# Kernel optimization log

Measured on AMD Instinct MI355X. Metric: run time of the kernel, lower is better.

Reference implementation:

```python
import jax, jax.numpy as jnp
import numpy as np

K = 1024
D = 256
BETA = 0.25


def setup_inputs() -> dict:
    key = jax.random.key(0)
    k1, k2 = jax.random.split(key)
    latents = jax.random.normal(k1, (32, D, 32, 32), dtype=jnp.float32)
    # nn.Embedding init: uniform(-1/K, 1/K)
    embedding = jax.random.uniform(k2, (K, D), dtype=jnp.float32,
                                   minval=-1.0 / K, maxval=1.0 / K)
    return {"latents": latents, "embedding": embedding}


def reference(latents, embedding):
    # latents: [B, D, H, W] -> [B, H, W, D]
    x = jnp.transpose(latents, (0, 2, 3, 1))
    input_shape = x.shape
    flat = x.reshape(-1, D)  # [N, D]

    # squared-L2 distances to codebook: [N, K]
    distances = (jnp.sum(flat ** 2, axis=1, keepdims=True)
                 + jnp.sum(embedding ** 2, axis=1)
                 - 2.0 * flat @ embedding.T)
    encoding_indices = jnp.argmin(distances, axis=1)  # [N]

    # one-hot encodings (returned output); quantize via direct gather
    encodings = jax.nn.one_hot(encoding_indices, K, dtype=latents.dtype)  # [N, K]
    quantized = embedding[encoding_indices].reshape(input_shape)  # [B, H, W, D]

    e_latent_loss = jnp.mean((jax.lax.stop_gradient(quantized) - x) ** 2)
    q_latent_loss = jnp.mean((quantized - jax.lax.stop_gradient(x)) ** 2)
    loss = q_latent_loss + BETA * e_latent_loss

    # straight-through estimator
    quantized_st = x + jax.lax.stop_gradient(quantized - x)

    avg_probs = jnp.mean(encodings, axis=0)  # [K]
    perplexity = jnp.exp(-jnp.sum(avg_probs * jnp.log(avg_probs + 1e-10)))

    return (loss,
            jnp.transpose(quantized_st, (0, 3, 1, 2)),  # [B, D, H, W]
            perplexity,
            encodings)
```

## Files before the change

kernel.cpp:

```cpp
#include <hip/hip_runtime.h>
#include <stdint.h>
#include <math.h>

typedef float  f32x4 __attribute__((ext_vector_type(4)));
typedef float  f32x2 __attribute__((ext_vector_type(2)));
typedef short  s16x8 __attribute__((ext_vector_type(8)));
typedef short  s16x4 __attribute__((ext_vector_type(4)));

#define KC   1024
#define DD   256
#define NR   32768

#define WS_HIST   0
#define WS_ACC    4096
#define WS_E2     8192
#define WS_IDX    12288
#define WS_PANEL  143360

#define ENC_OFF   8388610ULL

#define A_OFF   0
#define B_OFF   32768
#define E2_OFF  49152
#define SMEM_SZ 53248

#define GLD16(gp, lp) __builtin_amdgcn_global_load_lds(                      \
    (const __attribute__((address_space(1))) uint32_t*)(gp),                 \
    (__attribute__((address_space(3))) uint32_t*)(lp), 16, 0, 0)

__device__ __forceinline__ short f2bf(float f) {
    uint32_t u = __builtin_bit_cast(uint32_t, f);
    uint32_t r = (u + 0x7FFFu + ((u >> 16) & 1u)) >> 16;
    return (short)r;
}

__global__ void k_prep(const float* __restrict__ emb, char* __restrict__ ws) {
    int tid = threadIdx.x;
    if (blockIdx.x == 0) {
        uint32_t* hist = (uint32_t*)(ws + WS_HIST);
        #pragma unroll
        for (int j = 0; j < 4; j++) hist[tid * 4 + j] = 0u;
        if (tid < 2) ((float*)(ws + WS_ACC))[tid] = 0.f;
    }
    int wid = tid >> 6, lane = tid & 63;
    int code = blockIdx.x * 4 + wid;
    const float* row = emb + (size_t)code * DD;
    f32x4 v = *(const f32x4*)(row + lane * 4);
    s16x4 b;
    b[0] = f2bf(v.x); b[1] = f2bf(v.y); b[2] = f2bf(v.z); b[3] = f2bf(v.w);
    *(s16x4*)((short*)(ws + WS_PANEL) + (size_t)code * DD + lane * 4) = b;
    float ss = v.x * v.x + v.y * v.y + v.z * v.z + v.w * v.w;
    #pragma unroll
    for (int off = 1; off < 64; off <<= 1) ss += __shfl_xor(ss, off);
    if (lane == 0) ((float*)(ws + WS_E2))[code] = ss;
}

__global__ __launch_bounds__(256, 3) void k_argmin(const float* __restrict__ latents,
                                                   char* __restrict__ ws) {
    const char*  panelb = (const char*)(ws + WS_PANEL);
    const float* e2g    = (const float*)(ws + WS_E2);
    uint32_t*    hist   = (uint32_t*)(ws + WS_HIST);
    float*       acc    = (float*)(ws + WS_ACC);
    int*         idxo   = (int*)(ws + WS_IDX);

    __shared__ __align__(16) char smem[SMEM_SZ];

    int t    = threadIdx.x;
    int lane = t & 63;
    int wid  = t >> 6;
    int g    = lane >> 4, r16 = lane & 15;
    int nbase  = blockIdx.x * 128;
    int b      = nbase >> 10;
    int hwbase = nbase & 1023;

    #pragma unroll
    for (int i = 0; i < 2; i++) {
        uint32_t off = i * 4096 + wid * 1024;
        uint32_t so  = off + lane * 16;
        uint32_t ssw = so ^ (((so >> 9) & 7u) << 4);
        GLD16(panelb + ssw, smem + B_OFF + off);
    }
    {
        f32x4 ev = *(const f32x4*)(e2g + t * 4);
        *(f32x4*)(smem + E2_OFF + t * 16) = ev;
    }

    float xs = 0.f;
    s16x8 af[2][8];
    int rg = (t & 15) * 4;
    int dp = (t >> 4) * 2;
    int wb = 4 * ((t >> 4) & 3);

    #pragma unroll
    for (int h = 0; h < 2; h++) {
        const float* base = latents + (size_t)b * 262144 + hwbase + h * 64 + rg;
        #pragma unroll
        for (int i = 0; i < 8; i++) {
            int d = dp + i * 32;
            f32x4 v0 = *(const f32x4*)(base + (size_t)d * 1024);
            f32x4 v1 = *(const f32x4*)(base + (size_t)(d + 1) * 1024);
            xs += v0.x*v0.x + v0.y*v0.y + v0.z*v0.z + v0.w*v0.w;
            xs += v1.x*v1.x + v1.y*v1.y + v1.z*v1.z + v1.w*v1.w;
            int qb = d >> 3;
            #pragma unroll
            for (int q = 0; q < 4; q++) {
                int slot = rg + q;
                uint32_t pk = (uint32_t)(uint16_t)f2bf(v0[q])
                            | ((uint32_t)(uint16_t)f2bf(v1[q]) << 16);
                int quad = qb ^ (slot & 7);
                *(uint32_t*)(smem + A_OFF + slot * 512 + quad * 16 + wb) = pk;
            }
        }
        __syncthreads();
        if ((wid >> 1) == h) {
            int slotbase = (wid & 1) * 32;
            #pragma unroll
            for (int rt = 0; rt < 2; rt++) {
                #pragma unroll
                for (int kt = 0; kt < 8; kt++) {
                    int slot = slotbase + rt * 16 + r16;
                    int quad = (kt * 4 + g) ^ (slot & 7);
                    af[rt][kt] = *(const s16x8*)(smem + A_OFF + slot * 512 + quad * 16);
                }
            }
        }
        __syncthreads();
    }
    #pragma unroll
    for (int off = 1; off < 64; off <<= 1) xs += __shfl_xor(xs, off);
    if (lane == 0) atomicAdd(acc + 0, xs);
    __syncthreads();

    float vmin[2][4];
    int   vidx[2][4];
    #pragma unroll
    for (int rt = 0; rt < 2; rt++)
        #pragma unroll
        for (int j = 0; j < 4; j++) { vmin[rt][j] = 3.4e38f; vidx[rt][j] = 0; }

    const float* E2l = (const float*)(smem + E2_OFF);
    int cur = 0;
    for (int c = 0; c < 64; ++c) {
        if (c < 63) {
            size_t srcc = (size_t)(c + 1) * 8192;
            #pragma unroll
            for (int i = 0; i < 2; i++) {
                uint32_t off = i * 4096 + wid * 1024;
                uint32_t so  = off + lane * 16;
                uint32_t ssw = so ^ (((so >> 9) & 7u) << 4);
                GLD16(panelb + srcc + ssw, smem + B_OFF + (cur ^ 1) * 8192 + off);
            }
        }
        int cbase = c * 16;
        float e2c = E2l[cbase + r16];
        const char* Bc = smem + B_OFF + cur * 8192;
        s16x8 bf[8];
        #pragma unroll
        for (int kt = 0; kt < 8; kt++) {
            uint32_t byte = (uint32_t)(r16 * 512) + (((uint32_t)(kt * 64 + g * 16)) ^ (((uint32_t)(r16 & 7)) << 4));
            bf[kt] = *(const s16x8*)(Bc + byte);
        }
        #pragma unroll
        for (int rt = 0; rt < 2; rt++) {
            f32x4 a4 = {0.f, 0.f, 0.f, 0.f};
            #pragma unroll
            for (int kt = 0; kt < 8; kt++)
                a4 = __builtin_amdgcn_mfma_f32_16x16x32_bf16(af[rt][kt], bf[kt], a4, 0, 0, 0);
            #pragma unroll
            for (int j = 0; j < 4; j++) {
                float s = e2c - 2.f * a4[j];
                bool better = s < vmin[rt][j];
                vmin[rt][j] = better ? s : vmin[rt][j];
                vidx[rt][j] = better ? (cbase + r16) : vidx[rt][j];
            }
        }
        __syncthreads();
        cur ^= 1;
    }

    float minsum = 0.f;
    #pragma unroll
    for (int rt = 0; rt < 2; rt++) {
        #pragma unroll
        for (int j = 0; j < 4; j++) {
            float s = vmin[rt][j]; int ii = vidx[rt][j];
            #pragma unroll
            for (int off = 1; off < 16; off <<= 1) {
                float os = __shfl_xor(s, off);
                int   oi = __shfl_xor(ii, off);
                if (os < s || (os == s && oi < ii)) { s = os; ii = oi; }
            }
            minsum += s;
            if (r16 == 0) {
                int n = nbase + wid * 32 + rt * 16 + g * 4 + j;
                idxo[n] = ii;
                atomicAdd(hist + ii, 1u);
            }
        }
    }
    minsum += __shfl_xor(minsum, 16);
    minsum += __shfl_xor(minsum, 32);
    if (lane == 0) atomicAdd(acc + 1, minsum);
}

__global__ void k_quant(const float* __restrict__ emb, const char* __restrict__ ws,
                        float* __restrict__ out) {
    const int* idx = (const int*)(ws + WS_IDX);
    int tid = threadIdx.x;
    int dg  = blockIdx.x & 63;
    int hwt = (blockIdx.x >> 6) & 3;
    int b   = blockIdx.x >> 8;
    int hw  = hwt * 256 + tid;
    int n   = b * 1024 + hw;
    int code = idx[n];
    f32x4 v = *(const f32x4*)(emb + (size_t)code * 256 + dg * 4);
    float* dst = out + 1 + (size_t)b * 262144 + (size_t)dg * 4096 + hw;
    dst[0] = v.x; dst[1024] = v.y; dst[2048] = v.z; dst[3072] = v.w;
}

__global__ void k_onehot(const char* __restrict__ ws, float* __restrict__ out) {
    const int* idx = (const int*)(ws + WS_IDX);
    __shared__ int lidx[8];
    int tid = threadIdx.x;
    int rbase = blockIdx.x * 8;
    if (tid < 8) lidx[tid] = idx[rbase + tid];
    __syncthreads();
    f32x2* enc = (f32x2*)(out + ENC_OFF);
    #pragma unroll
    for (int j = 0; j < 16; j++) {
        int linear = j * 256 + tid;
        int rl = linear >> 9, c2 = linear & 511;
        int id = lidx[rl];
        f32x2 v;
        v.x = (2 * c2     == id) ? 1.f : 0.f;
        v.y = (2 * c2 + 1 == id) ? 1.f : 0.f;
        enc[(size_t)(rbase + rl) * 512 + c2] = v;
    }
}

__global__ void k_final(const char* __restrict__ ws, float* __restrict__ out) {
    __shared__ float red[256];
    const uint32_t* hist = (const uint32_t*)(ws + WS_HIST);
    const float*    acc  = (const float*)(ws + WS_ACC);
    int tid = threadIdx.x;
    float part = 0.f;
    #pragma unroll
    for (int j = 0; j < 4; j++) {
        float p = (float)hist[tid * 4 + j] * (1.f / 32768.f);
        part += p * logf(p + 1e-10f);
    }
    red[tid] = part;
    __syncthreads();
    for (int s = 128; s > 0; s >>= 1) {
        if (tid < s) red[tid] += red[tid + s];
        __syncthreads();
    }
    if (tid == 0) {
        out[8388609] = expf(-red[0]);
        out[0] = 1.25f * (acc[0] + acc[1]) * (1.f / 8388608.f);
    }
}

extern "C" void kernel_launch(void* const* d_in, const int* in_sizes, int n_in,
                              void* d_out, int out_size, void* d_ws, size_t ws_size,
                              hipStream_t stream) {
    const float* latents = (const float*)d_in[0];
    const float* emb     = (const float*)d_in[1];
    float* out = (float*)d_out;
    char*  ws  = (char*)d_ws;

    hipLaunchKernelGGL(k_prep,   dim3(256),  dim3(256), 0, stream, emb, ws);
    hipLaunchKernelGGL(k_argmin, dim3(256),  dim3(256), 0, stream, latents, ws);
    hipLaunchKernelGGL(k_quant,  dim3(8192), dim3(256), 0, stream, emb, ws, out);
    hipLaunchKernelGGL(k_onehot, dim3(4096), dim3(256), 0, stream, ws, out);
    hipLaunchKernelGGL(k_final,  dim3(1),    dim3(256), 0, stream, ws, out);
}
```

Before: 109.8 us.

## Split argmin codebook scan across two blocks and combine partial minima

Doubles the argmin grid by giving each block half of the codebook for its 128 rows. Each block writes its partial (min distance, index) pairs to workspace, and a new combine kernel picks the winner, writes the indices, histogram and min-sum. This aims to fill more compute units and shorten the serial codebook loop per block. The cost is that latent rows are loaded and converted twice, plus an extra kernel launch and partial-result traffic.

```diff
diff --git a/kernel.cpp b/kernel.cpp
--- a/kernel.cpp
+++ b/kernel.cpp
@@ -16,13 +16,14 @@
 #define WS_E2     8192
 #define WS_IDX    12288
 #define WS_PANEL  143360
+#define WS_PART   671744
 
 #define ENC_OFF   8388610ULL
 
 #define A_OFF   0
 #define B_OFF   32768
 #define E2_OFF  49152
-#define SMEM_SZ 53248
+#define SMEM_SZ 51200
 
 #define GLD16(gp, lp) __builtin_amdgcn_global_load_lds(                      \
     (const __attribute__((address_space(1))) uint32_t*)(gp),                 \
@@ -55,33 +56,34 @@
     if (lane == 0) ((float*)(ws + WS_E2))[code] = ss;
 }
 
-__global__ __launch_bounds__(256, 3) void k_argmin(const float* __restrict__ latents,
+__global__ __launch_bounds__(256, 2) void k_argmin(const float* __restrict__ latents,
                                                    char* __restrict__ ws) {
     const char*  panelb = (const char*)(ws + WS_PANEL);
     const float* e2g    = (const float*)(ws + WS_E2);
-    uint32_t*    hist   = (uint32_t*)(ws + WS_HIST);
     float*       acc    = (float*)(ws + WS_ACC);
-    int*         idxo   = (int*)(ws + WS_IDX);
 
     __shared__ __align__(16) char smem[SMEM_SZ];
 
-    int t    = threadIdx.x;
-    int lane = t & 63;
-    int wid  = t >> 6;
-    int g    = lane >> 4, r16 = lane & 15;
-    int nbase  = blockIdx.x * 128;
+    int t     = threadIdx.x;
+    int lane  = t & 63;
+    int wid   = t >> 6;
+    int g     = lane >> 4, r16 = lane & 15;
+    int rowgrp = blockIdx.x >> 1;
+    int chalf  = blockIdx.x & 1;
+    int nbase  = rowgrp * 128;
     int b      = nbase >> 10;
     int hwbase = nbase & 1023;
+    const char* pbase = panelb + (size_t)chalf * 262144;
 
     #pragma unroll
     for (int i = 0; i < 2; i++) {
         uint32_t off = i * 4096 + wid * 1024;
         uint32_t so  = off + lane * 16;
         uint32_t ssw = so ^ (((so >> 9) & 7u) << 4);
-        GLD16(panelb + ssw, smem + B_OFF + off);
-    }
-    {
-        f32x4 ev = *(const f32x4*)(e2g + t * 4);
+        GLD16(pbase + ssw, smem + B_OFF + off);
+    }
+    if (t < 128) {
+        f32x4 ev = *(const f32x4*)(e2g + chalf * 512 + t * 4);
         *(f32x4*)(smem + E2_OFF + t * 16) = ev;
     }
 
@@ -126,9 +128,11 @@
         }
         __syncthreads();
     }
-    #pragma unroll
-    for (int off = 1; off < 64; off <<= 1) xs += __shfl_xor(xs, off);
-    if (lane == 0) atomicAdd(acc + 0, xs);
+    if (chalf == 0) {
+        #pragma unroll
+        for (int off = 1; off < 64; off <<= 1) xs += __shfl_xor(xs, off);
+        if (lane == 0) atomicAdd(acc + 0, xs);
+    }
     __syncthreads();
 
     float vmin[2][4];
@@ -140,15 +144,16 @@
 
     const float* E2l = (const float*)(smem + E2_OFF);
     int cur = 0;
-    for (int c = 0; c < 64; ++c) {
-        if (c < 63) {
+    int codeglob = chalf * 512;
+    for (int c = 0; c < 32; ++c) {
+        if (c < 31) {
             size_t srcc = (size_t)(c + 1) * 8192;
             #pragma unroll
             for (int i = 0; i < 2; i++) {
                 uint32_t off = i * 4096 + wid * 1024;
                 uint32_t so  = off + lane * 16;
                 uint32_t ssw = so ^ (((so >> 9) & 7u) << 4);
-                GLD16(panelb + srcc + ssw, smem + B_OFF + (cur ^ 1) * 8192 + off);
+                GLD16(pbase + srcc + ssw, smem + B_OFF + (cur ^ 1) * 8192 + off);
             }
         }
         int cbase = c * 16;
@@ -171,14 +176,14 @@
                 float s = e2c - 2.f * a4[j];
                 bool better = s < vmin[rt][j];
                 vmin[rt][j] = better ? s : vmin[rt][j];
-                vidx[rt][j] = better ? (cbase + r16) : vidx[rt][j];
+                vidx[rt][j] = better ? (codeglob + cbase + r16) : vidx[rt][j];
             }
         }
         __syncthreads();
         cur ^= 1;
     }
 
-    float minsum = 0.f;
+    uint2* part = (uint2*)(ws + WS_PART) + (size_t)chalf * NR;
     #pragma unroll
     for (int rt = 0; rt < 2; rt++) {
         #pragma unroll
@@ -190,17 +195,34 @@
                 int   oi = __shfl_xor(ii, off);
                 if (os < s || (os == s && oi < ii)) { s = os; ii = oi; }
             }
-            minsum += s;
             if (r16 == 0) {
                 int n = nbase + wid * 32 + rt * 16 + g * 4 + j;
-                idxo[n] = ii;
-                atomicAdd(hist + ii, 1u);
-            }
-        }
-    }
-    minsum += __shfl_xor(minsum, 16);
-    minsum += __shfl_xor(minsum, 32);
-    if (lane == 0) atomicAdd(acc + 1, minsum);
+                uint2 pv;
+                pv.x = __builtin_bit_cast(uint32_t, s);
+                pv.y = (uint32_t)ii;
+                part[n] = pv;
+            }
+        }
+    }
+}
+
+__global__ void k_comb(char* __restrict__ ws) {
+    const uint2* part = (const uint2*)(ws + WS_PART);
+    uint32_t* hist = (uint32_t*)(ws + WS_HIST);
+    float*    acc  = (float*)(ws + WS_ACC);
+    int*      idxo = (int*)(ws + WS_IDX);
+    int n = blockIdx.x * 256 + threadIdx.x;
+    uint2 p0 = part[n];
+    uint2 p1 = part[NR + n];
+    float s0 = __builtin_bit_cast(float, p0.x);
+    float s1 = __builtin_bit_cast(float, p1.x);
+    float s = (s1 < s0) ? s1 : s0;
+    int  ii = (s1 < s0) ? (int)p1.y : (int)p0.y;
+    idxo[n] = ii;
+    atomicAdd(hist + ii, 1u);
+    #pragma unroll
+    for (int off = 1; off < 64; off <<= 1) s += __shfl_xor(s, off);
+    if ((threadIdx.x & 63) == 0) atomicAdd(acc + 1, s);
 }
 
 __global__ void k_quant(const float* __restrict__ emb, const char* __restrict__ ws,
@@ -270,7 +292,8 @@
     char*  ws  = (char*)d_ws;
 
     hipLaunchKernelGGL(k_prep,   dim3(256),  dim3(256), 0, stream, emb, ws);
-    hipLaunchKernelGGL(k_argmin, dim3(256),  dim3(256), 0, stream, latents, ws);
+    hipLaunchKernelGGL(k_argmin, dim3(512),  dim3(256), 0, stream, latents, ws);
+    hipLaunchKernelGGL(k_comb,   dim3(128),  dim3(256), 0, stream, ws);
     hipLaunchKernelGGL(k_quant,  dim3(8192), dim3(256), 0, stream, emb, ws, out);
     hipLaunchKernelGGL(k_onehot, dim3(4096), dim3(256), 0, stream, ws, out);
     hipLaunchKernelGGL(k_final,  dim3(1),    dim3(256), 0, stream, ws, out);
```

New measurement: 94.29 us. 14.1% less time.

## Split codebook across waves, load B fragments directly from global with register double-buffering

Applied to the files above, without the earlier changes.

The argmin kernel now handles 64 rows per block across 512 blocks instead of 128 rows across 256 blocks. Each pair of waves shares 32 rows and the codebook is split in half between the two waves, with a shared-memory reduction merging their partial argmins. The LDS-staged, barrier-synchronised codebook pipeline is replaced by direct global (L2) loads into registers, double-buffered in software. This removes per-chunk __syncthreads and LDS traffic and doubles the grid, at the cost of more global/L2 load traffic and higher register pressure (launch bounds lowered to 2).

```diff
diff --git a/kernel.cpp b/kernel.cpp
--- a/kernel.cpp
+++ b/kernel.cpp
@@ -20,13 +20,8 @@
 #define ENC_OFF   8388610ULL
 
 #define A_OFF   0
-#define B_OFF   32768
-#define E2_OFF  49152
-#define SMEM_SZ 53248
-
-#define GLD16(gp, lp) __builtin_amdgcn_global_load_lds(                      \
-    (const __attribute__((address_space(1))) uint32_t*)(gp),                 \
-    (__attribute__((address_space(3))) uint32_t*)(lp), 16, 0, 0)
+#define E2_OFF  32768
+#define SMEM_SZ 36864
 
 __device__ __forceinline__ short f2bf(float f) {
     uint32_t u = __builtin_bit_cast(uint32_t, f);
@@ -55,13 +50,13 @@
     if (lane == 0) ((float*)(ws + WS_E2))[code] = ss;
 }
 
-__global__ __launch_bounds__(256, 3) void k_argmin(const float* __restrict__ latents,
+__global__ __launch_bounds__(256, 2) void k_argmin(const float* __restrict__ latents,
                                                    char* __restrict__ ws) {
-    const char*  panelb = (const char*)(ws + WS_PANEL);
-    const float* e2g    = (const float*)(ws + WS_E2);
-    uint32_t*    hist   = (uint32_t*)(ws + WS_HIST);
-    float*       acc    = (float*)(ws + WS_ACC);
-    int*         idxo   = (int*)(ws + WS_IDX);
+    const short* panel = (const short*)(ws + WS_PANEL);
+    const float* e2g   = (const float*)(ws + WS_E2);
+    uint32_t*    hist  = (uint32_t*)(ws + WS_HIST);
+    float*       acc   = (float*)(ws + WS_ACC);
+    int*         idxo  = (int*)(ws + WS_IDX);
 
     __shared__ __align__(16) char smem[SMEM_SZ];
 
@@ -69,31 +64,18 @@
     int lane = t & 63;
     int wid  = t >> 6;
     int g    = lane >> 4, r16 = lane & 15;
-    int nbase  = blockIdx.x * 128;
+    int nbase  = blockIdx.x * 64;
     int b      = nbase >> 10;
     int hwbase = nbase & 1023;
 
-    #pragma unroll
-    for (int i = 0; i < 2; i++) {
-        uint32_t off = i * 4096 + wid * 1024;
-        uint32_t so  = off + lane * 16;
-        uint32_t ssw = so ^ (((so >> 9) & 7u) << 4);
-        GLD16(panelb + ssw, smem + B_OFF + off);
-    }
+    *(f32x4*)(smem + E2_OFF + t * 16) = *(const f32x4*)(e2g + t * 4);
+
+    float xs = 0.f;
     {
-        f32x4 ev = *(const f32x4*)(e2g + t * 4);
-        *(f32x4*)(smem + E2_OFF + t * 16) = ev;
-    }
-
-    float xs = 0.f;
-    s16x8 af[2][8];
-    int rg = (t & 15) * 4;
-    int dp = (t >> 4) * 2;
-    int wb = 4 * ((t >> 4) & 3);
-
-    #pragma unroll
-    for (int h = 0; h < 2; h++) {
-        const float* base = latents + (size_t)b * 262144 + hwbase + h * 64 + rg;
+        int rg = (t & 15) * 4;
+        int dp = (t >> 4) * 2;
+        int wb = 4 * ((t >> 4) & 3);
+        const float* base = latents + (size_t)b * 262144 + hwbase + rg;
         #pragma unroll
         for (int i = 0; i < 8; i++) {
             int d = dp + i * 32;
@@ -111,25 +93,23 @@
                 *(uint32_t*)(smem + A_OFF + slot * 512 + quad * 16 + wb) = pk;
             }
         }
-        __syncthreads();
-        if ((wid >> 1) == h) {
-            int slotbase = (wid & 1) * 32;
-            #pragma unroll
-            for (int rt = 0; rt < 2; rt++) {
-                #pragma unroll
-                for (int kt = 0; kt < 8; kt++) {
-                    int slot = slotbase + rt * 16 + r16;
-                    int quad = (kt * 4 + g) ^ (slot & 7);
-                    af[rt][kt] = *(const s16x8*)(smem + A_OFF + slot * 512 + quad * 16);
-                }
-            }
+        #pragma unroll
+        for (int off = 1; off < 64; off <<= 1) xs += __shfl_xor(xs, off);
+        if (lane == 0) atomicAdd(acc + 0, xs);
+    }
+    __syncthreads();
+
+    s16x8 af[2][8];
+    int rowoff = (wid >> 1) * 32;
+    #pragma unroll
+    for (int rt = 0; rt < 2; rt++) {
+        #pragma unroll
+        for (int kt = 0; kt < 8; kt++) {
+            int slot = rowoff + rt * 16 + r16;
+            int quad = (kt * 4 + g) ^ (slot & 7);
+            af[rt][kt] = *(const s16x8*)(smem + A_OFF + slot * 512 + quad * 16);
         }
-        __syncthreads();
-    }
-    #pragma unroll
-    for (int off = 1; off < 64; off <<= 1) xs += __shfl_xor(xs, off);
-    if (lane == 0) atomicAdd(acc + 0, xs);
-    __syncthreads();
+    }
 
     float vmin[2][4];
     int   vidx[2][4];
@@ -139,46 +119,50 @@
         for (int j = 0; j < 4; j++) { vmin[rt][j] = 3.4e38f; vidx[rt][j] = 0; }
 
     const float* E2l = (const float*)(smem + E2_OFF);
-    int cur = 0;
-    for (int c = 0; c < 64; ++c) {
-        if (c < 63) {
-            size_t srcc = (size_t)(c + 1) * 8192;
-            #pragma unroll
-            for (int i = 0; i < 2; i++) {
-                uint32_t off = i * 4096 + wid * 1024;
-                uint32_t so  = off + lane * 16;
-                uint32_t ssw = so ^ (((so >> 9) & 7u) << 4);
-                GLD16(panelb + srcc + ssw, smem + B_OFF + (cur ^ 1) * 8192 + off);
-            }
-        }
-        int cbase = c * 16;
-        float e2c = E2l[cbase + r16];
-        const char* Bc = smem + B_OFF + cur * 8192;
-        s16x8 bf[8];
-        #pragma unroll
-        for (int kt = 0; kt < 8; kt++) {
-            uint32_t byte = (uint32_t)(r16 * 512) + (((uint32_t)(kt * 64 + g * 16)) ^ (((uint32_t)(r16 & 7)) << 4));
-            bf[kt] = *(const s16x8*)(Bc + byte);
-        }
-        #pragma unroll
-        for (int rt = 0; rt < 2; rt++) {
-            f32x4 a4 = {0.f, 0.f, 0.f, 0.f};
-            #pragma unroll
-            for (int kt = 0; kt < 8; kt++)
-                a4 = __builtin_amdgcn_mfma_f32_16x16x32_bf16(af[rt][kt], bf[kt], a4, 0, 0, 0);
-            #pragma unroll
-            for (int j = 0; j < 4; j++) {
-                float s = e2c - 2.f * a4[j];
-                bool better = s < vmin[rt][j];
-                vmin[rt][j] = better ? s : vmin[rt][j];
-                vidx[rt][j] = better ? (cbase + r16) : vidx[rt][j];
-            }
-        }
-        __syncthreads();
-        cur ^= 1;
-    }
-
-    float minsum = 0.f;
+    int codebase = (wid & 1) * 512;
+    const short* prowbase = panel + (size_t)(codebase + r16) * DD + g * 8;
+
+#define LOADB(dst, cc) do {                                                   \
+        const s16x8* _p = (const s16x8*)(prowbase + (size_t)(cc) * 4096);     \
+        _Pragma("unroll")                                                     \
+        for (int kt = 0; kt < 8; kt++) dst[kt] = _p[kt * 4];                  \
+    } while (0)
+
+#define DOMFMA(bf, cc) do {                                                   \
+        int cb = codebase + (cc) * 16;                                        \
+        float e2c = E2l[cb + r16];                                            \
+        _Pragma("unroll")                                                     \
+        for (int rt = 0; rt < 2; rt++) {                                      \
+            f32x4 a4 = {0.f, 0.f, 0.f, 0.f};                                  \
+            _Pragma("unroll")                                                 \
+            for (int kt = 0; kt < 8; kt++)                                    \
+                a4 = __builtin_amdgcn_mfma_f32_16x16x32_bf16(af[rt][kt],      \
+                                                             bf[kt], a4, 0, 0, 0); \
+            _Pragma("unroll")                                                 \
+            for (int j = 0; j < 4; j++) {                                     \
+                float s = e2c - 2.f * a4[j];                                  \
+                bool better = s < vmin[rt][j];                                \
+                vmin[rt][j] = better ? s : vmin[rt][j];                       \
+                vidx[rt][j] = better ? (cb + r16) : vidx[rt][j];              \
+            }                                                                 \
+        }                                                                     \
+    } while (0)
+
+    s16x8 bfC[8], bfN[8];
+    LOADB(bfC, 0);
+    #pragma unroll 1
+    for (int c = 0; c < 32; c += 2) {
+        LOADB(bfN, c + 1);
+        DOMFMA(bfC, c);
+        if (c + 2 < 32) LOADB(bfC, c + 2);
+        DOMFMA(bfN, c + 1);
+    }
+#undef LOADB
+#undef DOMFMA
+
+    __syncthreads();
+    float* Lf = (float*)smem;
+    int*   Li = (int*)smem + 128;
     #pragma unroll
     for (int rt = 0; rt < 2; rt++) {
         #pragma unroll
@@ -190,17 +174,31 @@
                 int   oi = __shfl_xor(ii, off);
                 if (os < s || (os == s && oi < ii)) { s = os; ii = oi; }
             }
-            minsum += s;
             if (r16 == 0) {
-                int n = nbase + wid * 32 + rt * 16 + g * 4 + j;
-                idxo[n] = ii;
-                atomicAdd(hist + ii, 1u);
+                int row = rt * 16 + g * 4 + j;
+                Lf[wid * 32 + row] = s;
+                Li[wid * 32 + row] = ii;
             }
         }
     }
-    minsum += __shfl_xor(minsum, 16);
-    minsum += __shfl_xor(minsum, 32);
-    if (lane == 0) atomicAdd(acc + 1, minsum);
+    __syncthreads();
+
+    if (t < 64) {
+        int rh  = t >> 5;
+        int row = t & 31;
+        float s0 = Lf[(rh * 2) * 32 + row];
+        float s1 = Lf[(rh * 2 + 1) * 32 + row];
+        int   i0 = Li[(rh * 2) * 32 + row];
+        int   i1 = Li[(rh * 2 + 1) * 32 + row];
+        float s = (s1 < s0) ? s1 : s0;
+        int  ii = (s1 < s0) ? i1 : i0;
+        int n = nbase + rh * 32 + row;
+        idxo[n] = ii;
+        atomicAdd(hist + ii, 1u);
+        #pragma unroll
+        for (int off = 1; off < 64; off <<= 1) s += __shfl_xor(s, off);
+        if (t == 0) atomicAdd(acc + 1, s);
+    }
 }
 
 __global__ void k_quant(const float* __restrict__ emb, const char* __restrict__ ws,
@@ -270,7 +268,7 @@
     char*  ws  = (char*)d_ws;
 
     hipLaunchKernelGGL(k_prep,   dim3(256),  dim3(256), 0, stream, emb, ws);
-    hipLaunchKernelGGL(k_argmin, dim3(256),  dim3(256), 0, stream, latents, ws);
+    hipLaunchKernelGGL(k_argmin, dim3(512),  dim3(256), 0, stream, latents, ws);
     hipLaunchKernelGGL(k_quant,  dim3(8192), dim3(256), 0, stream, emb, ws, out);
     hipLaunchKernelGGL(k_onehot, dim3(4096), dim3(256), 0, stream, ws, out);
     hipLaunchKernelGGL(k_final,  dim3(1),    dim3(256), 0, stream, ws, out);
```

Measured after the change: 133.3 us. 21.4% more time.
